# Kernel optimization log

Hardware: AMD Instinct MI355X
Metric: run time of the kernel (lower is better)

## Reference

```python
import jax, jax.numpy as jnp
import numpy as np

B, L, H, E = 8, 1024, 8, 64  # self-attention: S=L, D=E
SCALE = 1.0 / np.sqrt(E).astype(np.float32)


def setup_inputs() -> dict:
    key = jax.random.key(0)
    ks = jax.random.split(key, 6)
    shp = (B, L, H, E)
    names = ["q_re", "q_im", "k_re", "k_im", "v_re", "v_im"]
    return {n: jax.random.normal(k, shp, dtype=jnp.float32) for n, k in zip(names, ks)}


def reference(q_re, q_im, k_re, k_im, v_re, v_im):
    q = jax.lax.complex(q_re, q_im)  # [B,L,H,E] complex64
    k = jax.lax.complex(k_re, k_im)  # [B,S,H,E] complex64
    # complex QK^T (no conjugate, matching torch einsum semantics)
    scores = jnp.einsum('blhe,bshe->bhls', q, k)      # [B,H,L,S] complex64
    A = jax.nn.softmax(SCALE * jnp.abs(scores), axis=-1)  # [B,H,L,S] real
    # A is promoted to complex with zero imaginary part in the original;
    # multiplying complex V by a real A is equivalent per real/imag part.
    V_re = jnp.einsum('bhls,bshd->blhd', A, v_re)     # [B,L,H,D]
    V_im = jnp.einsum('bhls,bshd->blhd', A, v_im)     # [B,L,H,D]
    return jnp.stack([V_re, V_im], axis=-1)           # [B,L,H,D,2] (re, im)
```

## Files before the change

### kernel.cpp

```cpp
#include <hip/hip_runtime.h>


#define B_ 8
#define L_ 1024
#define H_ 8
#define E_ 64
#define SB 64
#define QB 128
#define NT 16
#define IMG_BYTES 32768
#define WS_NEEDED (64ull * NT * IMG_BYTES)
#define C_EXP 0.18033688011112042f

typedef float  f32x4  __attribute__((ext_vector_type(4)));
typedef float  f32x16 __attribute__((ext_vector_type(16)));
typedef __bf16 bf16x8 __attribute__((ext_vector_type(8)));
typedef unsigned short u16x8 __attribute__((ext_vector_type(8)));
typedef unsigned short u16x4 __attribute__((ext_vector_type(4)));
typedef unsigned int   u32x4 __attribute__((ext_vector_type(4)));

static __device__ __forceinline__ unsigned short f2b(float f) {
    __bf16 h = (__bf16)f;
    return __builtin_bit_cast(unsigned short, h);
}

static __device__ __forceinline__ float fsqrt_(float x) {
    return __builtin_amdgcn_sqrtf(x);
}
static __device__ __forceinline__ float fexp2_(float x) {
    return __builtin_amdgcn_exp2f(x);
}

static __device__ __forceinline__ u16x8 pack8(float4 a, float4 b) {
    u16x8 t;
    t[0]=f2b(a.x); t[1]=f2b(a.y); t[2]=f2b(a.z); t[3]=f2b(a.w);
    t[4]=f2b(b.x); t[5]=f2b(b.y); t[6]=f2b(b.z); t[7]=f2b(b.w);
    return t;
}

static __device__ __forceinline__ f32x16 mfma32(u16x8 a, u16x8 b, f32x16 c) {
    return __builtin_amdgcn_mfma_f32_32x32x16_bf16(
        __builtin_bit_cast(bf16x8, a), __builtin_bit_cast(bf16x8, b), c, 0, 0, 0);
}

static __device__ __forceinline__ unsigned int cvtpk(float lo, float hi) {
    unsigned int r;
    asm("v_cvt_pk_bf16_f32 %0, %1, %2" : "=v"(r) : "v"(lo), "v"(hi));
    return r;
}

static __device__ __forceinline__ void plswap(unsigned int& x, unsigned int& y) {
    asm("v_permlane32_swap_b32 %0, %1" : "+v"(x), "+v"(y));
}

static __device__ __forceinline__ u16x8 negbf8(u16x8 a) {
    u32x4 u = __builtin_bit_cast(u32x4, a);
    u[0] ^= 0x80008000u; u[1] ^= 0x80008000u; u[2] ^= 0x80008000u; u[3] ^= 0x80008000u;
    return __builtin_bit_cast(u16x8, u);
}

__global__ __launch_bounds__(256) void ffa_prepack(
    const float* __restrict__ k_re, const float* __restrict__ k_im,
    const float* __restrict__ v_re, const float* __restrict__ v_im,
    char* __restrict__ ws)
{
    const int tid = threadIdx.x;
    const int bh  = blockIdx.x >> 4;
    const int st  = blockIdx.x & 15;
    const int b   = bh >> 3;
    const int h   = bh & 7;
    const int s0  = st * SB;
    char* const img = ws + (size_t)blockIdx.x * IMG_BYTES;

    const int l   = tid & 63;
    const int fg  = tid >> 6;
    const int l31 = l & 31;
    const int lh  = l >> 5;

#pragma unroll
    for (int ff = 0; ff < 8; ++ff) {
        const int f = fg * 8 + ff;
        u16x8 val;
        if (f < 16) {
            const int kh = f >> 3, ks = (f >> 1) & 3, c = f & 1;
            const float* src = (c ? k_im : k_re)
                + ((size_t)((b * L_ + s0 + kh * 32 + l31) * H_ + h)) * E_ + ks * 16 + lh * 8;
            const float4* p = (const float4*)src;
            val = pack8(p[0], p[1]);
        } else {
            const int g = f - 16, ks = g >> 2, j = g & 3;
            const float* src = (j >= 2) ? v_im : v_re;
            const int d = (j & 1) * 32 + l31;
            const int sb = s0 + ks * 16 + lh * 8;
            float4 t0, t1;
            t0.x = src[((size_t)((b * L_ + sb + 0) * H_ + h)) * E_ + d];
            t0.y = src[((size_t)((b * L_ + sb + 1) * H_ + h)) * E_ + d];
            t0.z = src[((size_t)((b * L_ + sb + 2) * H_ + h)) * E_ + d];
            t0.w = src[((size_t)((b * L_ + sb + 3) * H_ + h)) * E_ + d];
            t1.x = src[((size_t)((b * L_ + sb + 4) * H_ + h)) * E_ + d];
            t1.y = src[((size_t)((b * L_ + sb + 5) * H_ + h)) * E_ + d];
            t1.z = src[((size_t)((b * L_ + sb + 6) * H_ + h)) * E_ + d];
            t1.w = src[((size_t)((b * L_ + sb + 7) * H_ + h)) * E_ + d];
            val = pack8(t0, t1);
        }
        *(u16x8*)(img + f * 1024 + l * 16) = val;
    }
}

__global__ __launch_bounds__(256, 2) void ffa_main(
    const float* __restrict__ q_re, const float* __restrict__ q_im,
    const char* __restrict__ ws, float* __restrict__ out)
{
    const int tid  = threadIdx.x;
    const int lane = tid & 63;
    const int w    = tid >> 6;
    const int l31  = lane & 31;
    const int h    = lane >> 5;

    const int work = (blockIdx.x & 7) * 64 + (blockIdx.x >> 3);
    const int bh   = work >> 3;
    const int qblk = work & 7;
    const int b    = bh >> 3;
    const int hh   = bh & 7;
    const char* const imgs = ws + (size_t)bh * (NT * IMG_BYTES) + lane * 16;

    u16x8 qre[4], qim[4];
    {
        const int qrow = qblk * QB + w * 32 + l31;
        const int base = ((b * L_ + qrow) * H_ + hh) * E_;
#pragma unroll
        for (int ks = 0; ks < 4; ++ks) {
            const float4* pr = (const float4*)(q_re + base + ks * 16 + h * 8);
            const float4* pi = (const float4*)(q_im + base + ks * 16 + h * 8);
            qre[ks] = pack8(pr[0], pr[1]);
            qim[ks] = pack8(pi[0], pi[1]);
        }
    }

    f32x16 oR0 = {}, oR1 = {}, oI0 = {}, oI1 = {};
    float lsum = 0.f;
    const f32x16 z16 = {};

    for (int st = 0; st < NT; ++st) {
        const char* const tb = imgs + st * IMG_BYTES;

        u16x8 kf[16];
#pragma unroll
        for (int f = 0; f < 16; ++f)
            kf[f] = *(const u16x8*)(tb + f * 1024);

        u16x8 pa[4];
        u16x8 vf[16];

#pragma unroll
        for (int kh = 0; kh < 2; ++kh) {
            const u16x8* K = kf + kh * 8;
            u16x8 qn0 = negbf8(qim[0]), qn1 = negbf8(qim[1]);
            u16x8 qn2 = negbf8(qim[2]), qn3 = negbf8(qim[3]);

            __builtin_amdgcn_s_setprio(1);
            f32x16 sR0 = mfma32(K[0], qre[0], z16);
            f32x16 sI0 = mfma32(K[1], qre[0], z16);
            f32x16 sR1 = mfma32(K[4], qre[2], z16);
            f32x16 sI1 = mfma32(K[5], qre[2], z16);
            sR0 = mfma32(K[1], qn0,    sR0);
            sI0 = mfma32(K[0], qim[0], sI0);
            sR1 = mfma32(K[5], qn2,    sR1);
            sI1 = mfma32(K[4], qim[2], sI1);
            sR0 = mfma32(K[2], qre[1], sR0);
            sI0 = mfma32(K[3], qre[1], sI0);
            sR1 = mfma32(K[6], qre[3], sR1);
            sI1 = mfma32(K[7], qre[3], sI1);
            sR0 = mfma32(K[3], qn1,    sR0);
            sI0 = mfma32(K[2], qim[1], sI0);
            sR1 = mfma32(K[7], qn3,    sR1);
            sI1 = mfma32(K[6], qim[3], sI1);
            __builtin_amdgcn_s_setprio(0);

            if (kh == 0) {
#pragma unroll
                for (int g = 0; g < 8; ++g)
                    vf[g] = *(const u16x8*)(tb + (16 + g) * 1024);
            } else {
#pragma unroll
                for (int g = 8; g < 16; ++g)
                    vf[g] = *(const u16x8*)(tb + (16 + g) * 1024);
            }

            float p[16];
#pragma unroll
            for (int r = 0; r < 16; ++r) {
                float re = sR0[r] + sR1[r];
                float im = sI0[r] + sI1[r];
                float mag = fsqrt_(fmaf(re, re, im * im));
                p[r] = fexp2_(mag * C_EXP);
            }
            lsum += (((p[0]+p[1])+(p[2]+p[3])) + ((p[4]+p[5])+(p[6]+p[7])))
                  + (((p[8]+p[9])+(p[10]+p[11])) + ((p[12]+p[13])+(p[14]+p[15])));

            unsigned int a0 = cvtpk(p[0],  p[1]),  a1 = cvtpk(p[4],  p[5]);
            unsigned int a2 = cvtpk(p[2],  p[3]),  a3 = cvtpk(p[6],  p[7]);
            unsigned int b0 = cvtpk(p[8],  p[9]),  b1 = cvtpk(p[12], p[13]);
            unsigned int b2 = cvtpk(p[10], p[11]), b3 = cvtpk(p[14], p[15]);
            plswap(a0, a1);
            plswap(a2, a3);
            plswap(b0, b1);
            plswap(b2, b3);
            u32x4 wa = {a0, a2, a1, a3};
            u32x4 wb = {b0, b2, b1, b3};
            pa[2 * kh]     = __builtin_bit_cast(u16x8, wa);
            pa[2 * kh + 1] = __builtin_bit_cast(u16x8, wb);
        }

        __builtin_amdgcn_s_setprio(1);
#pragma unroll
        for (int ks = 0; ks < 4; ++ks) {
            oR0 = mfma32(pa[ks], vf[ks * 4 + 0], oR0);
            oR1 = mfma32(pa[ks], vf[ks * 4 + 1], oR1);
            oI0 = mfma32(pa[ks], vf[ks * 4 + 2], oI0);
            oI1 = mfma32(pa[ks], vf[ks * 4 + 3], oI1);
        }
        __builtin_amdgcn_s_setprio(0);
    }

    lsum += __shfl_xor(lsum, 32);
    const float inv = 1.0f / lsum;
#pragma unroll
    for (int r = 0; r < 16; ++r) {
        const int qs = (r & 3) + 8 * (r >> 2) + 4 * h;
        const float iv = __shfl(inv, qs);
        const int lq = qblk * QB + w * 32 + qs;
        float* op = out + ((b * L_ + lq) * H_ + hh) * (E_ * 2);
        float2 v0 = make_float2(oR0[r] * iv, oI0[r] * iv);
        float2 v1 = make_float2(oR1[r] * iv, oI1[r] * iv);
        *(float2*)(op + l31 * 2)      = v0;
        *(float2*)(op + 64 + l31 * 2) = v1;
    }
}

__global__ __launch_bounds__(256) void ffa_fwd_fb(
    const float* __restrict__ q_re, const float* __restrict__ q_im,
    const float* __restrict__ k_re, const float* __restrict__ k_im,
    const float* __restrict__ v_re, const float* __restrict__ v_im,
    float* __restrict__ out)
{
    __shared__ __align__(16) unsigned short Kt[64 * 128];
    __shared__ __align__(16) unsigned short Vt[128 * 64];
    __shared__ __align__(16) unsigned short Pw[4 * 16 * 64];
    char* const kb = (char*)Kt;
    char* const vb = (char*)Vt;

    const int tid  = threadIdx.x;
    const int lane = tid & 63;
    const int w    = tid >> 6;
    const int lr   = lane & 15;
    const int lg   = lane >> 4;
    const int lg16 = lg * 16;
    const int qblk = blockIdx.x & 15;
    const int bh   = blockIdx.x >> 4;
    const int b    = bh >> 3;
    const int h    = bh & 7;

    u16x8 qre[2], qim[2], qimn[2];
    {
        const int qrow = qblk * 64 + w * 16 + lr;
        const int base = ((b * L_ + qrow) * H_ + h) * E_ + lg * 8;
#pragma unroll
        for (int ks = 0; ks < 2; ++ks) {
            const float4* pr = (const float4*)(q_re + base + ks * 32);
            const float4* pi = (const float4*)(q_im + base + ks * 32);
            qre[ks] = pack8(pr[0], pr[1]);
            qim[ks] = pack8(pi[0], pi[1]);
#pragma unroll
            for (int i = 0; i < 8; ++i)
                qimn[ks][i] = (unsigned short)(qim[ks][i] ^ 0x8000u);
        }
    }

    float lsum[4];
    f32x4 Ore[4], Oim[4];
    const f32x4 zero = {0.f, 0.f, 0.f, 0.f};
#pragma unroll
    for (int r = 0; r < 4; ++r) lsum[r] = 0.f;
#pragma unroll
    for (int dt = 0; dt < 4; ++dt) { Ore[dt] = zero; Oim[dt] = zero; }

    const int sr = tid >> 2;
    const int sc = (tid & 3) * 16;
    const int vtens = tid >> 7;
    const int vd    = ((tid >> 4) & 7) * 8;
    const int vs    = (tid & 15) * 4;
    const float* const vsrc = vtens ? v_im : v_re;

    for (int st = 0; st < L_ / SB; ++st) {
        const int s0 = st * SB;
        {
            const int kg = ((b * L_ + s0 + sr) * H_ + h) * E_ + sc;
            const float4* pr = (const float4*)(k_re + kg);
            const float4* pi = (const float4*)(k_im + kg);
            float4 r0 = pr[0], r1 = pr[1], r2 = pr[2], r3 = pr[3];
            float4 i0 = pi[0], i1 = pi[1], i2 = pi[2], i3 = pi[3];
            const int krow = sr * 256;
            const int ksw  = (sr & 7) << 4;
            *(u16x8*)(kb + ((krow + sc * 2           ) ^ ksw)) = pack8(r0, r1);
            *(u16x8*)(kb + ((krow + sc * 2 + 16      ) ^ ksw)) = pack8(r2, r3);
            *(u16x8*)(kb + ((krow + 128 + sc * 2     ) ^ ksw)) = pack8(i0, i1);
            *(u16x8*)(kb + ((krow + 128 + sc * 2 + 16) ^ ksw)) = pack8(i2, i3);
        }
        {
            float vv[4][8];
#pragma unroll
            for (int j = 0; j < 4; ++j) {
                const float4* p = (const float4*)(vsrc + ((b * L_ + s0 + vs + j) * H_ + h) * E_ + vd);
                float4 x = p[0], y = p[1];
                vv[j][0]=x.x; vv[j][1]=x.y; vv[j][2]=x.z; vv[j][3]=x.w;
                vv[j][4]=y.x; vv[j][5]=y.y; vv[j][6]=y.z; vv[j][7]=y.w;
            }
#pragma unroll
            for (int i = 0; i < 8; ++i) {
                const int row = vtens * 64 + vd + i;
                u16x4 t;
                t[0]=f2b(vv[0][i]); t[1]=f2b(vv[1][i]); t[2]=f2b(vv[2][i]); t[3]=f2b(vv[3][i]);
                *(u16x4*)(vb + ((row * 128 + vs * 2) ^ ((row & 7) << 4))) = t;
            }
        }
        __syncthreads();

        f32x4 aR[4], aI[4];
#pragma unroll
        for (int t = 0; t < 4; ++t) { aR[t] = zero; aI[t] = zero; }
#pragma unroll
        for (int t = 0; t < 4; ++t) {
            const int key = t * 16 + lr;
            const char* kr = kb + key * 256;
            const int sw = (key & 7) << 4;
            u16x8 br0 = *(const u16x8*)(kr + (( lg16      ) ^ sw));
            u16x8 br1 = *(const u16x8*)(kr + (( 64 + lg16 ) ^ sw));
            u16x8 bi0 = *(const u16x8*)(kr + ((128 + lg16 ) ^ sw));
            u16x8 bi1 = *(const u16x8*)(kr + ((192 + lg16 ) ^ sw));
            aR[t] = __builtin_amdgcn_mfma_f32_16x16x32_bf16(__builtin_bit_cast(bf16x8,qre[0]),  __builtin_bit_cast(bf16x8,br0), aR[t],0,0,0);
            aR[t] = __builtin_amdgcn_mfma_f32_16x16x32_bf16(__builtin_bit_cast(bf16x8,qre[1]),  __builtin_bit_cast(bf16x8,br1), aR[t],0,0,0);
            aR[t] = __builtin_amdgcn_mfma_f32_16x16x32_bf16(__builtin_bit_cast(bf16x8,qimn[0]), __builtin_bit_cast(bf16x8,bi0), aR[t],0,0,0);
            aR[t] = __builtin_amdgcn_mfma_f32_16x16x32_bf16(__builtin_bit_cast(bf16x8,qimn[1]), __builtin_bit_cast(bf16x8,bi1), aR[t],0,0,0);
            aI[t] = __builtin_amdgcn_mfma_f32_16x16x32_bf16(__builtin_bit_cast(bf16x8,qre[0]),  __builtin_bit_cast(bf16x8,bi0), aI[t],0,0,0);
            aI[t] = __builtin_amdgcn_mfma_f32_16x16x32_bf16(__builtin_bit_cast(bf16x8,qre[1]),  __builtin_bit_cast(bf16x8,bi1), aI[t],0,0,0);
            aI[t] = __builtin_amdgcn_mfma_f32_16x16x32_bf16(__builtin_bit_cast(bf16x8,qim[0]),  __builtin_bit_cast(bf16x8,br0), aI[t],0,0,0);
            aI[t] = __builtin_amdgcn_mfma_f32_16x16x32_bf16(__builtin_bit_cast(bf16x8,qim[1]),  __builtin_bit_cast(bf16x8,br1), aI[t],0,0,0);
        }

        float p_[4][4];
#pragma unroll
        for (int t = 0; t < 4; ++t)
#pragma unroll
            for (int r = 0; r < 4; ++r) {
                float re = aR[t][r], im = aI[t][r];
                p_[t][r] = fexp2_(fsqrt_(fmaf(re, re, im * im)) * C_EXP);
            }
#pragma unroll
        for (int r = 0; r < 4; ++r)
            lsum[r] += (p_[0][r] + p_[1][r]) + (p_[2][r] + p_[3][r]);

        char* const pb = (char*)Pw + w * 2048;
#pragma unroll
        for (int t = 0; t < 4; ++t)
#pragma unroll
            for (int r = 0; r < 4; ++r) {
                const int prow = lg * 4 + r;
                *(unsigned short*)(pb + ((prow * 128 + (t * 16 + lr) * 2) ^ ((prow & 7) << 4)))
                    = f2b(p_[t][r]);
            }
        asm volatile("s_waitcnt lgkmcnt(0)" ::: "memory");
        __builtin_amdgcn_sched_barrier(0);
        const int psw = (lr & 7) << 4;
        u16x8 pf0 = *(const u16x8*)(pb + ((lr * 128 + lg16     ) ^ psw));
        u16x8 pf1 = *(const u16x8*)(pb + ((lr * 128 + 64 + lg16) ^ psw));

#pragma unroll
        for (int dt = 0; dt < 4; ++dt) {
            const int dr = dt * 16 + lr;
            const int swr = (dr & 7) << 4;
            const char* vrre = vb + dr * 128;
            const char* vrim = vb + (64 + dr) * 128;
            u16x8 vr0 = *(const u16x8*)(vrre + (( lg16     ) ^ swr));
            u16x8 vr1 = *(const u16x8*)(vrre + (( 64 + lg16) ^ swr));
            u16x8 vi0 = *(const u16x8*)(vrim + (( lg16     ) ^ swr));
            u16x8 vi1 = *(const u16x8*)(vrim + (( 64 + lg16) ^ swr));
            Ore[dt] = __builtin_amdgcn_mfma_f32_16x16x32_bf16(__builtin_bit_cast(bf16x8,pf0), __builtin_bit_cast(bf16x8,vr0), Ore[dt],0,0,0);
            Ore[dt] = __builtin_amdgcn_mfma_f32_16x16x32_bf16(__builtin_bit_cast(bf16x8,pf1), __builtin_bit_cast(bf16x8,vr1), Ore[dt],0,0,0);
            Oim[dt] = __builtin_amdgcn_mfma_f32_16x16x32_bf16(__builtin_bit_cast(bf16x8,pf0), __builtin_bit_cast(bf16x8,vi0), Oim[dt],0,0,0);
            Oim[dt] = __builtin_amdgcn_mfma_f32_16x16x32_bf16(__builtin_bit_cast(bf16x8,pf1), __builtin_bit_cast(bf16x8,vi1), Oim[dt],0,0,0);
        }
        __syncthreads();
    }

#pragma unroll
    for (int r = 0; r < 4; ++r) {
        float s = lsum[r];
        s += __shfl_xor(s, 1);
        s += __shfl_xor(s, 2);
        s += __shfl_xor(s, 4);
        s += __shfl_xor(s, 8);
        const float inv = 1.0f / s;
        const int lq = qblk * 64 + w * 16 + lg * 4 + r;
        const int obase = (((b * L_ + lq) * H_ + h) * E_) * 2;
#pragma unroll
        for (int dt = 0; dt < 4; ++dt) {
            const int d = dt * 16 + lr;
            float2 val = make_float2(Ore[dt][r] * inv, Oim[dt][r] * inv);
            *(float2*)(out + obase + d * 2) = val;
        }
    }
}

extern "C" void kernel_launch(void* const* d_in, const int* in_sizes, int n_in,
                              void* d_out, int out_size, void* d_ws, size_t ws_size,
                              hipStream_t stream) {
    const float* q_re = (const float*)d_in[0];
    const float* q_im = (const float*)d_in[1];
    const float* k_re = (const float*)d_in[2];
    const float* k_im = (const float*)d_in[3];
    const float* v_re = (const float*)d_in[4];
    const float* v_im = (const float*)d_in[5];
    float* out = (float*)d_out;

    if (ws_size >= WS_NEEDED) {
        char* ws = (char*)d_ws;
        hipLaunchKernelGGL(ffa_prepack, dim3(B_ * H_ * NT), dim3(256), 0, stream,
                           k_re, k_im, v_re, v_im, ws);
        hipLaunchKernelGGL(ffa_main, dim3(B_ * H_ * (L_ / QB)), dim3(256), 0, stream,
                           q_re, q_im, (const char*)ws, out);
    } else {
        hipLaunchKernelGGL(ffa_fwd_fb, dim3(B_ * H_ * (L_ / 64)), dim3(256), 0, stream,
                           q_re, q_im, k_re, k_im, v_re, v_im, out);
    }
}
```

Baseline: 90.48 us.

## Software-pipeline K/V fragment loads across half-tiles with sched barriers

Restructures the main loop so each 64-key tile is processed as two halves, with K fragments for the next half (and next tile) and V fragments for the current half issued before the compute of the current half, separated by scheduling barriers. The QK product is also reorganized into a single accumulator chain per half instead of two split accumulators summed later, cutting registers and add work. The intent is to hide global/L2 load latency behind MFMA and softmax work while lowering register pressure. The tradeoff is longer dependent MFMA chains per half and rigid scheduling imposed by the barriers.

Result: faster. 87.40 us (-3.4%).

```diff
diff --git a/kernel.cpp b/kernel.cpp
--- a/kernel.cpp
+++ b/kernel.cpp
@@ -57,6 +57,73 @@
     u32x4 u = __builtin_bit_cast(u32x4, a);
     u[0] ^= 0x80008000u; u[1] ^= 0x80008000u; u[2] ^= 0x80008000u; u[3] ^= 0x80008000u;
     return __builtin_bit_cast(u16x8, u);
+}
+
+static __device__ __forceinline__ void qk_half(
+    const u16x8 K[8], const u16x8 qre[4], const u16x8 qim[4],
+    f32x16& sR, f32x16& sI)
+{
+    const f32x16 z16 = {};
+    __builtin_amdgcn_s_setprio(1);
+    sR = mfma32(K[0], qre[0], z16);
+    sI = mfma32(K[1], qre[0], z16);
+    sR = mfma32(K[1], negbf8(qim[0]), sR);
+    sI = mfma32(K[0], qim[0], sI);
+    sR = mfma32(K[2], qre[1], sR);
+    sI = mfma32(K[3], qre[1], sI);
+    sR = mfma32(K[3], negbf8(qim[1]), sR);
+    sI = mfma32(K[2], qim[1], sI);
+    sR = mfma32(K[4], qre[2], sR);
+    sI = mfma32(K[5], qre[2], sI);
+    sR = mfma32(K[5], negbf8(qim[2]), sR);
+    sI = mfma32(K[4], qim[2], sI);
+    sR = mfma32(K[6], qre[3], sR);
+    sI = mfma32(K[7], qre[3], sI);
+    sR = mfma32(K[7], negbf8(qim[3]), sR);
+    sI = mfma32(K[6], qim[3], sI);
+    __builtin_amdgcn_s_setprio(0);
+}
+
+static __device__ __forceinline__ void sm_half(
+    f32x16 sR, f32x16 sI, float& lsum, u16x8& pa0, u16x8& pa1)
+{
+    float p[16];
+#pragma unroll
+    for (int r = 0; r < 16; ++r) {
+        float mag = fsqrt_(fmaf(sR[r], sR[r], sI[r] * sI[r]));
+        p[r] = fexp2_(mag * C_EXP);
+    }
+    lsum += (((p[0]+p[1])+(p[2]+p[3])) + ((p[4]+p[5])+(p[6]+p[7])))
+          + (((p[8]+p[9])+(p[10]+p[11])) + ((p[12]+p[13])+(p[14]+p[15])));
+
+    unsigned int a0 = cvtpk(p[0],  p[1]),  a1 = cvtpk(p[4],  p[5]);
+    unsigned int a2 = cvtpk(p[2],  p[3]),  a3 = cvtpk(p[6],  p[7]);
+    unsigned int b0 = cvtpk(p[8],  p[9]),  b1 = cvtpk(p[12], p[13]);
+    unsigned int b2 = cvtpk(p[10], p[11]), b3 = cvtpk(p[14], p[15]);
+    plswap(a0, a1);
+    plswap(a2, a3);
+    plswap(b0, b1);
+    plswap(b2, b3);
+    u32x4 wa = {a0, a2, a1, a3};
+    u32x4 wb = {b0, b2, b1, b3};
+    pa0 = __builtin_bit_cast(u16x8, wa);
+    pa1 = __builtin_bit_cast(u16x8, wb);
+}
+
+static __device__ __forceinline__ void pv_half(
+    u16x8 pa0, u16x8 pa1, const u16x8 vf[8],
+    f32x16& oR0, f32x16& oR1, f32x16& oI0, f32x16& oI1)
+{
+    __builtin_amdgcn_s_setprio(1);
+    oR0 = mfma32(pa0, vf[0], oR0);
+    oR1 = mfma32(pa0, vf[1], oR1);
+    oI0 = mfma32(pa0, vf[2], oI0);
+    oI1 = mfma32(pa0, vf[3], oI1);
+    oR0 = mfma32(pa1, vf[4], oR0);
+    oR1 = mfma32(pa1, vf[5], oR1);
+    oI0 = mfma32(pa1, vf[6], oI0);
+    oI1 = mfma32(pa1, vf[7], oI1);
+    __builtin_amdgcn_s_setprio(0);
 }
 
 __global__ __launch_bounds__(256) void ffa_prepack(
@@ -124,6 +191,12 @@
     const int hh   = bh & 7;
     const char* const imgs = ws + (size_t)bh * (NT * IMG_BYTES) + lane * 16;
 
+    u16x8 kc[8], kn[8], vf[8];
+#pragma unroll
+    for (int j = 0; j < 8; ++j)
+        kc[j] = *(const u16x8*)(imgs + j * 1024);
+    __builtin_amdgcn_sched_barrier(0);
+
     u16x8 qre[4], qim[4];
     {
         const int qrow = qblk * QB + w * 32 + l31;
@@ -139,88 +212,42 @@
 
     f32x16 oR0 = {}, oR1 = {}, oI0 = {}, oI1 = {};
     float lsum = 0.f;
-    const f32x16 z16 = {};
-
-    for (int st = 0; st < NT; ++st) {
-        const char* const tb = imgs + st * IMG_BYTES;
-
-        u16x8 kf[16];
-#pragma unroll
-        for (int f = 0; f < 16; ++f)
-            kf[f] = *(const u16x8*)(tb + f * 1024);
-
-        u16x8 pa[4];
-        u16x8 vf[16];
-
-#pragma unroll
-        for (int kh = 0; kh < 2; ++kh) {
-            const u16x8* K = kf + kh * 8;
-            u16x8 qn0 = negbf8(qim[0]), qn1 = negbf8(qim[1]);
-            u16x8 qn2 = negbf8(qim[2]), qn3 = negbf8(qim[3]);
-
-            __builtin_amdgcn_s_setprio(1);
-            f32x16 sR0 = mfma32(K[0], qre[0], z16);
-            f32x16 sI0 = mfma32(K[1], qre[0], z16);
-            f32x16 sR1 = mfma32(K[4], qre[2], z16);
-            f32x16 sI1 = mfma32(K[5], qre[2], z16);
-            sR0 = mfma32(K[1], qn0,    sR0);
-            sI0 = mfma32(K[0], qim[0], sI0);
-            sR1 = mfma32(K[5], qn2,    sR1);
-            sI1 = mfma32(K[4], qim[2], sI1);
-            sR0 = mfma32(K[2], qre[1], sR0);
-            sI0 = mfma32(K[3], qre[1], sI0);
-            sR1 = mfma32(K[6], qre[3], sR1);
-            sI1 = mfma32(K[7], qre[3], sI1);
-            sR0 = mfma32(K[3], qn1,    sR0);
-            sI0 = mfma32(K[2], qim[1], sI0);
-            sR1 = mfma32(K[7], qn3,    sR1);
-            sI1 = mfma32(K[6], qim[3], sI1);
-            __builtin_amdgcn_s_setprio(0);
-
-            if (kh == 0) {
-#pragma unroll
-                for (int g = 0; g < 8; ++g)
-                    vf[g] = *(const u16x8*)(tb + (16 + g) * 1024);
-            } else {
-#pragma unroll
-                for (int g = 8; g < 16; ++g)
-                    vf[g] = *(const u16x8*)(tb + (16 + g) * 1024);
-            }
-
-            float p[16];
-#pragma unroll
-            for (int r = 0; r < 16; ++r) {
-                float re = sR0[r] + sR1[r];
-                float im = sI0[r] + sI1[r];
-                float mag = fsqrt_(fmaf(re, re, im * im));
-                p[r] = fexp2_(mag * C_EXP);
-            }
-            lsum += (((p[0]+p[1])+(p[2]+p[3])) + ((p[4]+p[5])+(p[6]+p[7])))
-                  + (((p[8]+p[9])+(p[10]+p[11])) + ((p[12]+p[13])+(p[14]+p[15])));
-
-            unsigned int a0 = cvtpk(p[0],  p[1]),  a1 = cvtpk(p[4],  p[5]);
-            unsigned int a2 = cvtpk(p[2],  p[3]),  a3 = cvtpk(p[6],  p[7]);
-            unsigned int b0 = cvtpk(p[8],  p[9]),  b1 = cvtpk(p[12], p[13]);
-            unsigned int b2 = cvtpk(p[10], p[11]), b3 = cvtpk(p[14], p[15]);
-            plswap(a0, a1);
-            plswap(a2, a3);
-            plswap(b0, b1);
-            plswap(b2, b3);
-            u32x4 wa = {a0, a2, a1, a3};
-            u32x4 wb = {b0, b2, b1, b3};
-            pa[2 * kh]     = __builtin_bit_cast(u16x8, wa);
-            pa[2 * kh + 1] = __builtin_bit_cast(u16x8, wb);
-        }
-
-        __builtin_amdgcn_s_setprio(1);
-#pragma unroll
-        for (int ks = 0; ks < 4; ++ks) {
-            oR0 = mfma32(pa[ks], vf[ks * 4 + 0], oR0);
-            oR1 = mfma32(pa[ks], vf[ks * 4 + 1], oR1);
-            oI0 = mfma32(pa[ks], vf[ks * 4 + 2], oI0);
-            oI1 = mfma32(pa[ks], vf[ks * 4 + 3], oI1);
-        }
-        __builtin_amdgcn_s_setprio(0);
+
+    for (int t = 0; t < NT; ++t) {
+        const char* const tb0 = imgs + (size_t)t * IMG_BYTES;
+        const char* const tb1 = tb0 + IMG_BYTES;
+
+#pragma unroll
+        for (int g = 0; g < 8; ++g)
+            vf[g] = *(const u16x8*)(tb0 + (16 + g) * 1024);
+#pragma unroll
+        for (int j = 0; j < 8; ++j)
+            kn[j] = *(const u16x8*)(tb0 + 8192 + j * 1024);
+        __builtin_amdgcn_sched_barrier(0);
+        {
+            f32x16 sR, sI;
+            qk_half(kc, qre, qim, sR, sI);
+            u16x8 pa0, pa1;
+            sm_half(sR, sI, lsum, pa0, pa1);
+            pv_half(pa0, pa1, vf, oR0, oR1, oI0, oI1);
+        }
+
+#pragma unroll
+        for (int g = 0; g < 8; ++g)
+            vf[g] = *(const u16x8*)(tb0 + (24 + g) * 1024);
+        if (t < NT - 1) {
+#pragma unroll
+            for (int j = 0; j < 8; ++j)
+                kc[j] = *(const u16x8*)(tb1 + j * 1024);
+        }
+        __builtin_amdgcn_sched_barrier(0);
+        {
+            f32x16 sR, sI;
+            qk_half(kn, qre, qim, sR, sI);
+            u16x8 pa0, pa1;
+            sm_half(sR, sI, lsum, pa0, pa1);
+            pv_half(pa0, pa1, vf, oR0, oR1, oI0, oI1);
+        }
     }
 
     lsum += __shfl_xor(lsum, 32);
```
